# Performance work log

Hardware: AMD Instinct MI355X
Metric: run time of the kernel (lower is better)

## Reference

```python
import jax, jax.numpy as jnp
import numpy as np

ALPHA = 0.2  # LeakyReLU negative slope
NEG_INF = jnp.float32(-9e15)


def setup_inputs() -> dict:
    key = jax.random.key(0)
    k1, k2, k3, k4, k5, k6 = jax.random.split(key, 6)
    B, N, F_in, F_out = 8, 2048, 256, 64
    h = jax.random.normal(k1, (B, N, F_in), dtype=jnp.float32)
    adj = jax.random.randint(k2, (B, N, N), 0, 2, dtype=jnp.int32)
    level = jax.random.uniform(k3, (B, N), dtype=jnp.float32)
    node_type = jax.random.uniform(k4, (B, N, N), dtype=jnp.float32)
    W = jax.random.normal(k5, (F_in, F_out), dtype=jnp.float32) * 1.414 / np.sqrt(F_in)
    a = jax.random.normal(k6, (2 * F_out, 1), dtype=jnp.float32) * 1.414 / np.sqrt(2 * F_out)
    return {"h": h, "adj": adj, "level": level, "node_type": node_type, "W": W, "a": a}


def reference(h, adj, level, node_type, W, a):
    # h: [B,N,Fin], adj/node_type: [B,N,N], level: [B,N], W: [Fin,Fout], a: [2*Fout,1]
    F_out = W.shape[1]
    Wh = jnp.einsum('bnf,fo->bno', h, W)  # [B,N,Fout]
    # Additive attention decomposed: e[b,i,j] = a1.Wh_i + a2.Wh_j (no O(N^2*2F) tensor)
    a1 = a[:F_out, 0]
    a2 = a[F_out:, 0]
    f1 = Wh @ a1  # [B,N]
    f2 = Wh @ a2  # [B,N]
    e = jax.nn.leaky_relu(f1[:, :, None] + f2[:, None, :], negative_slope=ALPHA)  # [B,N,N]
    # gat_our=True path: node_type scales scores, level scales Wh
    e = e * node_type
    Wh = Wh * level[:, :, None]
    attention = jnp.where(adj > 0, e, NEG_INF)
    attention = jax.nn.softmax(attention, axis=1)  # faithful: original softmax over dim=1
    # dropout p=0 / eval mode -> identity
    h_prime = jnp.einsum('bij,bjo->bio', attention, Wh)  # [B,N,Fout]
    return jax.nn.relu(h_prime)  # concat=True
```

## Files before the change

### kernel.cpp

```cpp
#include <hip/hip_runtime.h>

#define BB 8
#define NN 2048
#define FIN 256
#define FO 64

typedef short short8_t __attribute__((ext_vector_type(8)));
typedef float float4_t __attribute__((ext_vector_type(4)));

__device__ __forceinline__ unsigned short f2bf(float x) {
  unsigned int u = __float_as_uint(x);
  unsigned int r = (u + 0x7fffu + ((u >> 16) & 1u)) >> 16;
  return (unsigned short)r;
}

__global__ __launch_bounds__(256) void k0_zero(float* __restrict__ scol) {
  scol[blockIdx.x * 256 + threadIdx.x] = 0.0f;
}

__global__ __launch_bounds__(256) void k1_gemm(
    const float* __restrict__ h,
    const float* __restrict__ level,
    const float* __restrict__ W,
    const float* __restrict__ a,
    float* __restrict__ V, float* __restrict__ f1, float* __restrict__ f2)
{
  __shared__ float hs[16 * 260];
  __shared__ float parts1[16 * 17];
  __shared__ float parts2[16 * 17];
  int t = threadIdx.x;
  int b = blockIdx.x >> 7;
  int i0 = (blockIdx.x & 127) * 16;

  {
    int r_ld = t >> 4, f0 = (t & 15) * 16;
    const float* hp = h + (size_t)(b * NN + i0 + r_ld) * FIN + f0;
    float4 x0 = *(const float4*)(hp);
    float4 x1 = *(const float4*)(hp + 4);
    float4 x2 = *(const float4*)(hp + 8);
    float4 x3 = *(const float4*)(hp + 12);
    float* hd = &hs[r_ld * 260 + f0];
    *(float4*)(hd + 0) = x0; *(float4*)(hd + 4) = x1;
    *(float4*)(hd + 8) = x2; *(float4*)(hd + 12) = x3;
  }
  __syncthreads();

  int r = t >> 4;
  int c4 = (t & 15) * 4;
  float4 acc = {0, 0, 0, 0};

  for (int f = 0; f < FIN; f += 8) {
    float4 hv0 = *(const float4*)&hs[r * 260 + f];
    float4 hv1 = *(const float4*)&hs[r * 260 + f + 4];
    float hvv[8] = {hv0.x, hv0.y, hv0.z, hv0.w, hv1.x, hv1.y, hv1.z, hv1.w};
    #pragma unroll
    for (int k = 0; k < 8; ++k) {
      float4 wv = *(const float4*)&W[(size_t)(f + k) * FO + c4];
      acc.x += hvv[k] * wv.x; acc.y += hvv[k] * wv.y;
      acc.z += hvv[k] * wv.z; acc.w += hvv[k] * wv.w;
    }
  }

  float p1 = acc.x * a[c4] + acc.y * a[c4 + 1] + acc.z * a[c4 + 2] + acc.w * a[c4 + 3];
  float p2 = acc.x * a[64 + c4] + acc.y * a[64 + c4 + 1] +
             acc.z * a[64 + c4 + 2] + acc.w * a[64 + c4 + 3];
  parts1[r * 17 + (t & 15)] = p1;
  parts2[r * 17 + (t & 15)] = p2;
  __syncthreads();
  if (t < 16) {
    float s1 = 0.f, s2 = 0.f;
    #pragma unroll
    for (int g = 0; g < 16; ++g) { s1 += parts1[t * 17 + g]; s2 += parts2[t * 17 + g]; }
    f1[b * NN + i0 + t] = s1;
    f2[b * NN + i0 + t] = s2;
  }

  float lv = level[b * NN + i0 + r];
  float4 vv = {acc.x * lv, acc.y * lv, acc.z * lv, acc.w * lv};
  *(float4*)&V[(size_t)(b * NN + i0 + r) * FO + c4] = vv;
}

template <int STORE_U>
__global__ __launch_bounds__(256) void k2a_stats(
    const int* __restrict__ adj,
    const float* __restrict__ ntp,
    const float* __restrict__ f1,
    const float* __restrict__ f2,
    unsigned short* __restrict__ u_bf,
    unsigned char* __restrict__ bits,
    float* __restrict__ scol)
{
  __shared__ float red[4 * 520];
  int t = threadIdx.x;
  int b = blockIdx.x >> 8;
  int i0 = (blockIdx.x & 255) * 8;
  int w = t >> 6, l = t & 63;

  #pragma unroll
  for (int c = 0; c < 4; ++c) {
    int j8 = c * 512 + l * 8;
    float4 f2lo = *(const float4*)(f2 + b * NN + j8);
    float4 f2hi = *(const float4*)(f2 + b * NN + j8 + 4);
    float f2v[8] = {f2lo.x, f2lo.y, f2lo.z, f2lo.w, f2hi.x, f2hi.y, f2hi.z, f2hi.w};
    float acc8[8] = {0, 0, 0, 0, 0, 0, 0, 0};

    #pragma unroll
    for (int r = 0; r < 2; ++r) {
      size_t base = (size_t)(b * NN + i0 + w * 2 + r);
      const int* ap = adj + base * NN + j8;
      int4 a0 = *(const int4*)ap;
      int4 a1 = *(const int4*)(ap + 4);
      const float* npp = ntp + base * NN + j8;
      float4 n0 = *(const float4*)npp;
      float4 n1 = *(const float4*)(npp + 4);
      float f1v = f1[base];
      float ntf[8] = {n0.x, n0.y, n0.z, n0.w, n1.x, n1.y, n1.z, n1.w};
      int am[8] = {a0.x, a0.y, a0.z, a0.w, a1.x, a1.y, a1.z, a1.w};
      float uv[8];
      unsigned int mb = 0;
      #pragma unroll
      for (int e = 0; e < 8; ++e) {
        float x = f1v + f2v[e];
        x = fmaxf(x, 0.2f * x);
        float E = x * ntf[e];
        bool m = am[e] > 0;
        float u = m ? __expf(E) : 0.0f;
        uv[e] = u;
        acc8[e] += u;
        mb |= (m ? 1u : 0u) << e;
      }
      if (STORE_U) {
        uint4 pk;
        pk.x = (unsigned int)f2bf(uv[0]) | ((unsigned int)f2bf(uv[1]) << 16);
        pk.y = (unsigned int)f2bf(uv[2]) | ((unsigned int)f2bf(uv[3]) << 16);
        pk.z = (unsigned int)f2bf(uv[4]) | ((unsigned int)f2bf(uv[5]) << 16);
        pk.w = (unsigned int)f2bf(uv[6]) | ((unsigned int)f2bf(uv[7]) << 16);
        *(uint4*)(u_bf + base * NN + j8) = pk;
      } else {
        bits[base * (NN / 8) + c * 64 + l] = (unsigned char)mb;
      }
    }

    #pragma unroll
    for (int e = 0; e < 8; ++e) red[w * 520 + l * 8 + e] = acc8[e];
    __syncthreads();
    {
      int j2 = t * 2;
      float s0 = 0.f, s1 = 0.f;
      #pragma unroll
      for (int ww = 0; ww < 4; ++ww) {
        float2 v = *(const float2*)&red[ww * 520 + j2];
        s0 += v.x; s1 += v.y;
      }
      atomicAdd(&scol[b * NN + c * 512 + j2], s0);
      atomicAdd(&scol[b * NN + c * 512 + j2 + 1], s1);
    }
    __syncthreads();
  }
}

__global__ __launch_bounds__(256) void k2b_pack(
    const float* __restrict__ V,
    const float* __restrict__ scol,
    unsigned short* __restrict__ vf)
{
  int t = threadIdx.x;
  int b = blockIdx.x >> 6;
  int kk = blockIdx.x & 63;
  int ng = t >> 6;
  int l = t & 63;
  int jb = kk * 32 + ((l >> 4) * 8);
  int o = ng * 16 + (l & 15);
  unsigned int pk[4];
  #pragma unroll
  for (int p = 0; p < 4; ++p) {
    int jr0 = jb + 2 * p, jr1 = jb + 2 * p + 1;
    float s0 = scol[b * NN + jr0];
    float s1 = scol[b * NN + jr1];
    float i0 = (s0 > 0.f) ? (1.0f / s0) : 0.0f;
    float i1 = (s1 > 0.f) ? (1.0f / s1) : 0.0f;
    float v0 = V[(size_t)(b * NN + jr0) * FO + o] * i0;
    float v1 = V[(size_t)(b * NN + jr1) * FO + o] * i1;
    pk[p] = (unsigned int)f2bf(v0) | ((unsigned int)f2bf(v1) << 16);
  }
  *(uint4*)(vf + (size_t)(((b * 64 + kk) * 4 + ng) * 64 + l) * 8) =
      make_uint4(pk[0], pk[1], pk[2], pk[3]);
}

__global__ __launch_bounds__(256) void k3_agg_u(
    const unsigned short* __restrict__ u_bf,
    const unsigned short* __restrict__ vf,
    float* __restrict__ outp)
{
  __shared__ float red[4 * 16 * 68];
  int t = threadIdx.x;
  int b = blockIdx.x >> 7;
  int i0 = (blockIdx.x & 127) * 16;
  int w = t >> 6, l = t & 63;
  int col = l & 15, quad = l >> 4;
  const unsigned short* urow = u_bf + (size_t)(b * NN + i0 + col) * NN + quad * 8;
  const unsigned short* vbase = vf + (size_t)(b * 64) * 2048 + l * 8;

  short8_t Aall[16];
  #pragma unroll
  for (int s = 0; s < 16; ++s)
    Aall[s] = *(const short8_t*)(urow + (size_t)(w * 16 + s) * 32);

  const unsigned short* vb0 = vbase + (size_t)(w * 16) * 2048;
  short8_t c0 = *(const short8_t*)(vb0);
  short8_t c1 = *(const short8_t*)(vb0 + 512);
  short8_t c2 = *(const short8_t*)(vb0 + 1024);
  short8_t c3 = *(const short8_t*)(vb0 + 1536);

  float4_t acc0 = {0, 0, 0, 0}, acc1 = {0, 0, 0, 0}, acc2 = {0, 0, 0, 0}, acc3 = {0, 0, 0, 0};

  #pragma unroll
  for (int s = 0; s < 16; ++s) {
    short8_t n0, n1, n2, n3;
    if (s < 15) {
      const unsigned short* vn = vbase + (size_t)(w * 16 + s + 1) * 2048;
      n0 = *(const short8_t*)(vn);
      n1 = *(const short8_t*)(vn + 512);
      n2 = *(const short8_t*)(vn + 1024);
      n3 = *(const short8_t*)(vn + 1536);
    }
    acc0 = __builtin_amdgcn_mfma_f32_16x16x32_bf16(Aall[s], c0, acc0, 0, 0, 0);
    acc1 = __builtin_amdgcn_mfma_f32_16x16x32_bf16(Aall[s], c1, acc1, 0, 0, 0);
    acc2 = __builtin_amdgcn_mfma_f32_16x16x32_bf16(Aall[s], c2, acc2, 0, 0, 0);
    acc3 = __builtin_amdgcn_mfma_f32_16x16x32_bf16(Aall[s], c3, acc3, 0, 0, 0);
    if (s < 15) { c0 = n0; c1 = n1; c2 = n2; c3 = n3; }
  }

  #pragma unroll
  for (int r = 0; r < 4; ++r) {
    int rowi = quad * 4 + r;
    red[w * 1088 + rowi * 68 + 0 + col] = acc0[r];
    red[w * 1088 + rowi * 68 + 16 + col] = acc1[r];
    red[w * 1088 + rowi * 68 + 32 + col] = acc2[r];
    red[w * 1088 + rowi * 68 + 48 + col] = acc3[r];
  }
  __syncthreads();

  int row = t >> 4, o4 = (t & 15) * 4;
  const float* rp = &red[row * 68 + o4];
  float4 s0 = *(const float4*)(rp);
  float4 s1 = *(const float4*)(rp + 1088);
  float4 s2 = *(const float4*)(rp + 2176);
  float4 s3 = *(const float4*)(rp + 3264);
  float4 o;
  o.x = fmaxf(s0.x + s1.x + s2.x + s3.x, 0.0f);
  o.y = fmaxf(s0.y + s1.y + s2.y + s3.y, 0.0f);
  o.z = fmaxf(s0.z + s1.z + s2.z + s3.z, 0.0f);
  o.w = fmaxf(s0.w + s1.w + s2.w + s3.w, 0.0f);
  *(float4*)&outp[(size_t)(b * NN + i0 + row) * FO + o4] = o;
}

__global__ __launch_bounds__(256) void k3_agg_b(
    const float* __restrict__ ntp,
    const unsigned char* __restrict__ bits,
    const float* __restrict__ f1,
    const float* __restrict__ f2,
    const unsigned short* __restrict__ vf,
    float* __restrict__ outp)
{
  __shared__ float red[4 * 16 * 68];
  int t = threadIdx.x;
  int b = blockIdx.x >> 7;
  int i0 = (blockIdx.x & 127) * 16;
  int w = t >> 6, l = t & 63;
  int col = l & 15, quad = l >> 4;
  int gi = b * NN + i0 + col;
  float f1v = f1[gi];
  const float* ntrow = ntp + (size_t)gi * NN;
  const unsigned char* brow = bits + (size_t)gi * (NN / 8);
  float4_t acc0 = {0, 0, 0, 0}, acc1 = {0, 0, 0, 0}, acc2 = {0, 0, 0, 0}, acc3 = {0, 0, 0, 0};

  for (int s = 0; s < 16; ++s) {
    int kk = w * 16 + s;
    int jq = kk * 32 + quad * 8;
    unsigned int m8 = brow[jq >> 3];
    float4 n0 = *(const float4*)(ntrow + jq);
    float4 n1 = *(const float4*)(ntrow + jq + 4);
    float4 g0 = *(const float4*)(f2 + b * NN + jq);
    float4 g1 = *(const float4*)(f2 + b * NN + jq + 4);
    float f2v[8] = {g0.x, g0.y, g0.z, g0.w, g1.x, g1.y, g1.z, g1.w};
    float ntf[8] = {n0.x, n0.y, n0.z, n0.w, n1.x, n1.y, n1.z, n1.w};
    union { unsigned int u[4]; short8_t v; } A;
    #pragma unroll
    for (int p = 0; p < 4; ++p) {
      int e0 = 2 * p, e1 = 2 * p + 1;
      float x0 = f1v + f2v[e0]; x0 = fmaxf(x0, 0.2f * x0);
      float u0 = ((m8 >> e0) & 1u) ? __expf(x0 * ntf[e0]) : 0.0f;
      float x1 = f1v + f2v[e1]; x1 = fmaxf(x1, 0.2f * x1);
      float u1 = ((m8 >> e1) & 1u) ? __expf(x1 * ntf[e1]) : 0.0f;
      A.u[p] = (unsigned int)f2bf(u0) | ((unsigned int)f2bf(u1) << 16);
    }
    const unsigned short* vb = vf + (size_t)(b * 64 + kk) * 2048 + l * 8;
    short8_t bf0 = *(const short8_t*)(vb);
    short8_t bf1 = *(const short8_t*)(vb + 512);
    short8_t bf2 = *(const short8_t*)(vb + 1024);
    short8_t bf3 = *(const short8_t*)(vb + 1536);
    acc0 = __builtin_amdgcn_mfma_f32_16x16x32_bf16(A.v, bf0, acc0, 0, 0, 0);
    acc1 = __builtin_amdgcn_mfma_f32_16x16x32_bf16(A.v, bf1, acc1, 0, 0, 0);
    acc2 = __builtin_amdgcn_mfma_f32_16x16x32_bf16(A.v, bf2, acc2, 0, 0, 0);
    acc3 = __builtin_amdgcn_mfma_f32_16x16x32_bf16(A.v, bf3, acc3, 0, 0, 0);
  }

  #pragma unroll
  for (int r = 0; r < 4; ++r) {
    int rowi = quad * 4 + r;
    red[w * 1088 + rowi * 68 + 0 + col] = acc0[r];
    red[w * 1088 + rowi * 68 + 16 + col] = acc1[r];
    red[w * 1088 + rowi * 68 + 32 + col] = acc2[r];
    red[w * 1088 + rowi * 68 + 48 + col] = acc3[r];
  }
  __syncthreads();

  int row = t >> 4, o4 = (t & 15) * 4;
  const float* rp = &red[row * 68 + o4];
  float4 s0 = *(const float4*)(rp);
  float4 s1 = *(const float4*)(rp + 1088);
  float4 s2 = *(const float4*)(rp + 2176);
  float4 s3 = *(const float4*)(rp + 3264);
  float4 o;
  o.x = fmaxf(s0.x + s1.x + s2.x + s3.x, 0.0f);
  o.y = fmaxf(s0.y + s1.y + s2.y + s3.y, 0.0f);
  o.z = fmaxf(s0.z + s1.z + s2.z + s3.z, 0.0f);
  o.w = fmaxf(s0.w + s1.w + s2.w + s3.w, 0.0f);
  *(float4*)&outp[(size_t)(b * NN + i0 + row) * FO + o4] = o;
}

extern "C" void kernel_launch(void* const* d_in, const int* in_sizes, int n_in,
                              void* d_out, int out_size, void* d_ws, size_t ws_size,
                              hipStream_t stream) {
  const float* h = (const float*)d_in[0];
  const int* adj = (const int*)d_in[1];
  const float* level = (const float*)d_in[2];
  const float* ntm = (const float*)d_in[3];
  const float* W = (const float*)d_in[4];
  const float* a = (const float*)d_in[5];
  float* outp = (float*)d_out;

  float* V = (float*)d_ws;
  float* f1 = V + (size_t)BB * NN * FO;
  float* f2 = f1 + BB * NN;
  float* scol = f2 + BB * NN;
  unsigned short* vf = (unsigned short*)(scol + BB * NN);
  char* tail = (char*)(vf + (size_t)BB * NN * FO);
  size_t fixed = (size_t)(tail - (char*)d_ws);
  size_t need_u = fixed + (size_t)BB * NN * NN * 2;
  bool big = (ws_size >= need_u);

  k0_zero<<<64, 256, 0, stream>>>(scol);
  k1_gemm<<<1024, 256, 0, stream>>>(h, level, W, a, V, f1, f2);
  if (big) {
    unsigned short* u_bf = (unsigned short*)tail;
    k2a_stats<1><<<2048, 256, 0, stream>>>(adj, ntm, f1, f2, u_bf, nullptr, scol);
    k2b_pack<<<512, 256, 0, stream>>>(V, scol, vf);
    k3_agg_u<<<1024, 256, 0, stream>>>(u_bf, vf, outp);
  } else {
    unsigned char* bits = (unsigned char*)tail;
    k2a_stats<0><<<2048, 256, 0, stream>>>(adj, ntm, f1, f2, nullptr, bits, scol);
    k2b_pack<<<512, 256, 0, stream>>>(V, scol, vf);
    k3_agg_b<<<1024, 256, 0, stream>>>(ntm, bits, f1, f2, vf, outp);
  }
}
```

Baseline: 379.8 us.

## Double-buffer adj/node_type tiles via async global-to-LDS loads; stage W in LDS

The stats kernel now streams adj and node_type rows into double-buffered LDS tiles using global_load_lds. The next chunk's load is issued while the current one is processed, aiming to hide the latency of the dominant N^2 memory traffic. Column mapping is rearranged so each lane handles strided columns, and the mask bits are built with a wavefront ballot. The projection GEMM kernel also stages W into shared memory in two halves instead of reading it from global memory for every FMA. Risks: correctness depends on the barrier waiting for the async LDS writes, and the u_bf store path drops from 16-byte to 2-byte stores.

After: 349.3 us. 1.09x faster.

```diff
diff --git a/kernel.cpp b/kernel.cpp
--- a/kernel.cpp
+++ b/kernel.cpp
@@ -13,6 +13,11 @@
   unsigned int r = (u + 0x7fffu + ((u >> 16) & 1u)) >> 16;
   return (unsigned short)r;
 }
+
+#define GLD16(gp, lp)                                                          \
+  __builtin_amdgcn_global_load_lds(                                            \
+      (const __attribute__((address_space(1))) void*)(gp),                     \
+      (__attribute__((address_space(3))) void*)(lp), 16, 0, 0)
 
 __global__ __launch_bounds__(256) void k0_zero(float* __restrict__ scol) {
   scol[blockIdx.x * 256 + threadIdx.x] = 0.0f;
@@ -25,6 +30,7 @@
     const float* __restrict__ a,
     float* __restrict__ V, float* __restrict__ f1, float* __restrict__ f2)
 {
+  __shared__ float wlds[128 * 64];
   __shared__ float hs[16 * 260];
   __shared__ float parts1[16 * 17];
   __shared__ float parts2[16 * 17];
@@ -43,21 +49,30 @@
     *(float4*)(hd + 0) = x0; *(float4*)(hd + 4) = x1;
     *(float4*)(hd + 8) = x2; *(float4*)(hd + 12) = x3;
   }
-  __syncthreads();
 
   int r = t >> 4;
   int c4 = (t & 15) * 4;
   float4 acc = {0, 0, 0, 0};
 
-  for (int f = 0; f < FIN; f += 8) {
-    float4 hv0 = *(const float4*)&hs[r * 260 + f];
-    float4 hv1 = *(const float4*)&hs[r * 260 + f + 4];
-    float hvv[8] = {hv0.x, hv0.y, hv0.z, hv0.w, hv1.x, hv1.y, hv1.z, hv1.w};
-    #pragma unroll
-    for (int k = 0; k < 8; ++k) {
-      float4 wv = *(const float4*)&W[(size_t)(f + k) * FO + c4];
-      acc.x += hvv[k] * wv.x; acc.y += hvv[k] * wv.y;
-      acc.z += hvv[k] * wv.z; acc.w += hvv[k] * wv.w;
+  #pragma unroll
+  for (int half = 0; half < 2; ++half) {
+    __syncthreads();
+    #pragma unroll
+    for (int q = 0; q < 8; ++q) {
+      int idx = q * 1024 + t * 4;
+      *(float4*)&wlds[idx] = *(const float4*)&W[half * 8192 + idx];
+    }
+    __syncthreads();
+    for (int f = 0; f < 128; f += 8) {
+      float4 hv0 = *(const float4*)&hs[r * 260 + half * 128 + f];
+      float4 hv1 = *(const float4*)&hs[r * 260 + half * 128 + f + 4];
+      float hvv[8] = {hv0.x, hv0.y, hv0.z, hv0.w, hv1.x, hv1.y, hv1.z, hv1.w};
+      #pragma unroll
+      for (int k = 0; k < 8; ++k) {
+        float4 wv = *(const float4*)&wlds[(f + k) * 64 + c4];
+        acc.x += hvv[k] * wv.x; acc.y += hvv[k] * wv.y;
+        acc.z += hvv[k] * wv.z; acc.w += hvv[k] * wv.w;
+      }
     }
   }
 
@@ -90,72 +105,73 @@
     unsigned char* __restrict__ bits,
     float* __restrict__ scol)
 {
-  __shared__ float red[4 * 520];
+  __shared__ int ladj[2][8 * 256];
+  __shared__ float lnt[2][8 * 256];
+  __shared__ float red[4 * 264];
   int t = threadIdx.x;
   int b = blockIdx.x >> 8;
   int i0 = (blockIdx.x & 255) * 8;
   int w = t >> 6, l = t & 63;
-
-  #pragma unroll
-  for (int c = 0; c < 4; ++c) {
-    int j8 = c * 512 + l * 8;
-    float4 f2lo = *(const float4*)(f2 + b * NN + j8);
-    float4 f2hi = *(const float4*)(f2 + b * NN + j8 + 4);
-    float f2v[8] = {f2lo.x, f2lo.y, f2lo.z, f2lo.w, f2hi.x, f2hi.y, f2hi.z, f2hi.w};
-    float acc8[8] = {0, 0, 0, 0, 0, 0, 0, 0};
-
+  size_t rbase = (size_t)(b * NN + i0);
+  int r0 = 2 * w;
+
+  auto stage = [&](int buf, int c) {
     #pragma unroll
     for (int r = 0; r < 2; ++r) {
-      size_t base = (size_t)(b * NN + i0 + w * 2 + r);
-      const int* ap = adj + base * NN + j8;
-      int4 a0 = *(const int4*)ap;
-      int4 a1 = *(const int4*)(ap + 4);
-      const float* npp = ntp + base * NN + j8;
-      float4 n0 = *(const float4*)npp;
-      float4 n1 = *(const float4*)(npp + 4);
-      float f1v = f1[base];
-      float ntf[8] = {n0.x, n0.y, n0.z, n0.w, n1.x, n1.y, n1.z, n1.w};
-      int am[8] = {a0.x, a0.y, a0.z, a0.w, a1.x, a1.y, a1.z, a1.w};
-      float uv[8];
-      unsigned int mb = 0;
+      int row = r0 + r;
+      const int* ga = adj + (rbase + row) * NN + c * 256 + l * 4;
+      const float* gn = ntp + (rbase + row) * NN + c * 256 + l * 4;
+      GLD16(ga, &ladj[buf][row * 256]);
+      GLD16(gn, &lnt[buf][row * 256]);
+    }
+  };
+
+  stage(0, 0);
+
+  float f1v0 = f1[rbase + r0];
+  float f1v1 = f1[rbase + r0 + 1];
+  float f2all[32];
+  #pragma unroll
+  for (int c = 0; c < 8; ++c)
+    #pragma unroll
+    for (int k = 0; k < 4; ++k)
+      f2all[c * 4 + k] = f2[b * NN + c * 256 + 64 * k + l];
+
+  for (int c = 0; c < 8; ++c) {
+    int cur = c & 1;
+    __syncthreads();
+
+    float acc4[4] = {0, 0, 0, 0};
+    #pragma unroll
+    for (int r = 0; r < 2; ++r) {
+      int row = r0 + r;
+      float f1v = r ? f1v1 : f1v0;
       #pragma unroll
-      for (int e = 0; e < 8; ++e) {
-        float x = f1v + f2v[e];
+      for (int k = 0; k < 4; ++k) {
+        int av = ladj[cur][row * 256 + 64 * k + l];
+        float nv = lnt[cur][row * 256 + 64 * k + l];
+        float x = f1v + f2all[c * 4 + k];
         x = fmaxf(x, 0.2f * x);
-        float E = x * ntf[e];
-        bool m = am[e] > 0;
-        float u = m ? __expf(E) : 0.0f;
-        uv[e] = u;
-        acc8[e] += u;
-        mb |= (m ? 1u : 0u) << e;
+        bool m = av > 0;
+        float u = m ? __expf(x * nv) : 0.0f;
+        acc4[k] += u;
+        if (STORE_U) {
+          u_bf[(rbase + row) * NN + c * 256 + 64 * k + l] = f2bf(u);
+        } else {
+          unsigned long long bal = __ballot(m);
+          if (l == 0)
+            *(unsigned long long*)&bits[(rbase + row) * (NN / 8) + c * 32 + k * 8] = bal;
+        }
       }
-      if (STORE_U) {
-        uint4 pk;
-        pk.x = (unsigned int)f2bf(uv[0]) | ((unsigned int)f2bf(uv[1]) << 16);
-        pk.y = (unsigned int)f2bf(uv[2]) | ((unsigned int)f2bf(uv[3]) << 16);
-        pk.z = (unsigned int)f2bf(uv[4]) | ((unsigned int)f2bf(uv[5]) << 16);
-        pk.w = (unsigned int)f2bf(uv[6]) | ((unsigned int)f2bf(uv[7]) << 16);
-        *(uint4*)(u_bf + base * NN + j8) = pk;
-      } else {
-        bits[base * (NN / 8) + c * 64 + l] = (unsigned char)mb;
-      }
-    }
-
-    #pragma unroll
-    for (int e = 0; e < 8; ++e) red[w * 520 + l * 8 + e] = acc8[e];
+    }
+    #pragma unroll
+    for (int k = 0; k < 4; ++k) red[w * 264 + 64 * k + l] = acc4[k];
     __syncthreads();
-    {
-      int j2 = t * 2;
-      float s0 = 0.f, s1 = 0.f;
-      #pragma unroll
-      for (int ww = 0; ww < 4; ++ww) {
-        float2 v = *(const float2*)&red[ww * 520 + j2];
-        s0 += v.x; s1 += v.y;
-      }
-      atomicAdd(&scol[b * NN + c * 512 + j2], s0);
-      atomicAdd(&scol[b * NN + c * 512 + j2 + 1], s1);
-    }
-    __syncthreads();
+
+    if (c < 7) stage(cur ^ 1, c + 1);
+
+    float s = red[0 * 264 + t % 256] + red[1 * 264 + t] + red[2 * 264 + t] + red[3 * 264 + t];
+    atomicAdd(&scol[b * NN + c * 256 + t], s);
   }
 }
 
```
